# Optimization experiments

Measured on AMD Instinct MI355X. Metric: run time of the kernel, lower is better.

The kernel has to match this reference:

```python
import jax, jax.numpy as jnp
import numpy as np

EMBED = 1024
HEADS = 16


def setup_inputs() -> dict:
    key = jax.random.key(0)
    k1, k2, k3 = jax.random.split(key, 3)
    B, S, D = 2, 2048, EMBED
    x = jax.random.normal(k1, (B, S, D), dtype=jnp.float32)
    # nn.Linear weights: stored as [out, in]; y = x @ W.T
    w_qkv = jax.random.normal(k2, (3 * D, D), dtype=jnp.float32) * (D ** -0.5)
    w_out = jax.random.normal(k3, (D, D), dtype=jnp.float32) * (D ** -0.5)
    return {"x": x, "w_qkv": w_qkv, "w_out": w_out}


def reference(x, w_qkv, w_out):
    B, S, D = x.shape
    H = HEADS
    hd = D // H
    qkv = x @ w_qkv.T                       # [B, S, 3D]
    q, k, v = jnp.split(qkv, 3, axis=-1)
    # 'b l (head k) -> b head l k'
    def heads(t):
        return t.reshape(B, S, H, hd).transpose(0, 2, 1, 3)
    q, k, v = heads(q), heads(k), heads(v)
    scale = hd ** 0.5
    scores = jnp.einsum('bhqd,bhkd->bhqk', q, k) / scale
    probs = jax.nn.softmax(scores, axis=-1)
    out = jnp.einsum('bhqk,bhkd->bhqd', probs, v)  # [B, H, S, hd]
    out = out.transpose(0, 2, 1, 3).reshape(B, S, D)
    return out @ w_out.T
```

## Files before the change

### kernel.cpp

```cpp
#include <hip/hip_runtime.h>

typedef short short8 __attribute__((ext_vector_type(8)));
typedef float floatx4 __attribute__((ext_vector_type(4)));
typedef unsigned short ushort_t;

#define EMBED 1024
#define HEADS 16
#define HD 64
#define SEQ 2048
#define BATCH 2

__device__ inline ushort_t f2bf(float f) {
    unsigned int u = __float_as_uint(f);
    u += 0x7fff + ((u >> 16) & 1);
    return (ushort_t)(u >> 16);
}

typedef const __attribute__((address_space(1))) unsigned int* gas_t;
typedef __attribute__((address_space(3))) unsigned int* las_t;
__device__ inline void async_copy16(const ushort_t* g, ushort_t* l) {
    __builtin_amdgcn_global_load_lds((gas_t)g, (las_t)l, 16, 0, 0);
}

__global__ void cast3_kernel(const float* __restrict__ a, ushort_t* __restrict__ oa, int na,
                             const float* __restrict__ b, ushort_t* __restrict__ ob, int nb,
                             const float* __restrict__ c, ushort_t* __restrict__ oc, int nc) {
    int idx = (blockIdx.x * blockDim.x + threadIdx.x) * 4;
    const float* in; ushort_t* out;
    if (idx < na)            { in = a;  out = oa; }
    else if (idx < na + nb)  { in = b;  out = ob; idx -= na; }
    else if (idx < na + nb + nc) { in = c; out = oc; idx -= na + nb; }
    else return;
    float4 f = *(const float4*)(in + idx);
    ushort4 o;
    o.x = f2bf(f.x); o.y = f2bf(f.y); o.z = f2bf(f.z); o.w = f2bf(f.w);
    *(ushort4*)(out + idx) = o;
}

#define BM 128
#define BN 128
#define BK 32

template<int MODE>
__launch_bounds__(256, 3)
__global__ void gemm_bt(const ushort_t* __restrict__ A, const ushort_t* __restrict__ B,
                        float* __restrict__ outF,
                        ushort_t* __restrict__ qb, ushort_t* __restrict__ kb,
                        ushort_t* __restrict__ vtb,
                        int M, int N, int K) {
    __shared__ ushort_t As[BM * BK];
    __shared__ ushort_t Bs[BN * BK];
    const int t    = threadIdx.x;
    const int lane = t & 63;
    const int wave = t >> 6;
    const int wm   = (wave >> 1) * 64;
    const int wn   = (wave & 1) * 64;
    const int m0   = blockIdx.y * BM;
    const int n0   = blockIdx.x * BN;
    const int col  = lane & 15;
    const int quad = lane >> 4;

    const int srow = lane >> 2;
    const int sgr  = (lane & 3) ^ (srow & 3);
    const int rslot = quad ^ (col & 3);

    floatx4 acc[4][4] = {};

    for (int k0 = 0; k0 < K; k0 += BK) {
        for (int half = 0; half < 2; ++half) {
            int row0 = wave * 32 + half * 16;
            int r = row0 + srow;
            async_copy16(A + (size_t)(m0 + r) * K + k0 + sgr * 8, &As[row0 * BK]);
            async_copy16(B + (size_t)(n0 + r) * K + k0 + sgr * 8, &Bs[row0 * BK]);
        }
        __syncthreads();
        short8 a[4], b[4];
        for (int i = 0; i < 4; ++i)
            a[i] = *(const short8*)(&As[(wm + i * 16 + col) * BK + rslot * 8]);
        for (int j = 0; j < 4; ++j)
            b[j] = *(const short8*)(&Bs[(wn + j * 16 + col) * BK + rslot * 8]);
        for (int i = 0; i < 4; ++i)
            for (int j = 0; j < 4; ++j)
                acc[i][j] = __builtin_amdgcn_mfma_f32_16x16x32_bf16(a[i], b[j], acc[i][j], 0, 0, 0);
        __syncthreads();
    }

    for (int i = 0; i < 4; ++i)
        for (int j = 0; j < 4; ++j)
            for (int r = 0; r < 4; ++r) {
                int m = m0 + wm + i * 16 + quad * 4 + r;
                int n = n0 + wn + j * 16 + col;
                float c = acc[i][j][r];
                if (MODE == 1) {
                    outF[(size_t)m * N + n] = c;
                } else {
                    int part = n >> 10;
                    int within = n & 1023;
                    int h = within >> 6, d = within & 63;
                    int bb = m >> 11, s = m & 2047;
                    ushort_t v = f2bf(c);
                    if (part == 0)      qb [(((size_t)bb * HEADS + h) * SEQ + s) * HD + d] = v;
                    else if (part == 1) kb [(((size_t)bb * HEADS + h) * SEQ + s) * HD + d] = v;
                    else                vtb[(((size_t)bb * HEADS + h) * HD + d) * SEQ + s] = v;
                }
            }
}

#define LDP 72

__launch_bounds__(256, 3)
__global__ void attn_kernel(const ushort_t* __restrict__ qb, const ushort_t* __restrict__ kb,
                            const ushort_t* __restrict__ vtb, ushort_t* __restrict__ attn) {
    __shared__ ushort_t Klds[2][64 * 64];
    __shared__ ushort_t Vlds[2][64 * 64];
    __shared__ ushort_t Plds[4][2][16 * LDP];
    const int t    = threadIdx.x;
    const int lane = t & 63;
    const int wave = t >> 6;
    const int col  = lane & 15;
    const int quad = lane >> 4;
    const int bh   = blockIdx.y;
    const int q0   = blockIdx.x * 128 + wave * 32;

    const ushort_t* Q  = qb  + (size_t)bh * SEQ * HD;
    const ushort_t* Kp = kb  + (size_t)bh * SEQ * HD;
    const ushort_t* Vt = vtb + (size_t)bh * HD * SEQ;

    const int srow = lane >> 3;
    const int sgr  = lane & 7;

    short8 qf[2][2];
    for (int qt = 0; qt < 2; ++qt) {
        qf[qt][0] = *(const short8*)(Q + (size_t)(q0 + qt * 16 + col) * HD + quad * 8);
        qf[qt][1] = *(const short8*)(Q + (size_t)(q0 + qt * 16 + col) * HD + 32 + quad * 8);
    }

    floatx4 acc[2][4] = {};
    float lsum[2] = {0.f, 0.f};
    const float SC = 0.125f * 1.44269504f;
    const int sw = col & 7;

    auto stage = [&](int kt, int buf) {
        for (int inst = 0; inst < 2; ++inst) {
            int row0 = wave * 16 + inst * 8;
            int r = row0 + srow;
            const ushort_t* gk = Kp + (size_t)(kt + r) * HD + ((sgr ^ (r & 7)) * 8);
            async_copy16(gk, &Klds[buf][row0 * 64]);
            const ushort_t* gv = Vt + (size_t)r * SEQ + kt + ((sgr ^ (r & 7)) * 8);
            async_copy16(gv, &Vlds[buf][row0 * 64]);
        }
    };

    stage(0, 0);
    __syncthreads();

    for (int kt = 0; kt < SEQ; kt += 64) {
        const int cur = (kt >> 6) & 1;
        stage((kt + 64) & (SEQ - 1), cur ^ 1);

        const ushort_t* Kc = Klds[cur];
        const ushort_t* Vc = Vlds[cur];

        short8 kf[4][2];
        for (int n = 0; n < 4; ++n) {
            int row = n * 16 + col;
            kf[n][0] = *(const short8*)(Kc + row * 64 + ((quad ^ sw) * 8));
            kf[n][1] = *(const short8*)(Kc + row * 64 + (((4 + quad) ^ sw) * 8));
        }
        for (int qt = 0; qt < 2; ++qt)
            for (int n = 0; n < 4; ++n) {
                floatx4 z = {};
                z = __builtin_amdgcn_mfma_f32_16x16x32_bf16(kf[n][0], qf[qt][0], z, 0, 0, 0);
                z = __builtin_amdgcn_mfma_f32_16x16x32_bf16(kf[n][1], qf[qt][1], z, 0, 0, 0);
                unsigned int u0 = __float_as_uint(__builtin_amdgcn_exp2f(z[0] * SC));
                unsigned int u1 = __float_as_uint(__builtin_amdgcn_exp2f(z[1] * SC));
                unsigned int u2 = __float_as_uint(__builtin_amdgcn_exp2f(z[2] * SC));
                unsigned int u3 = __float_as_uint(__builtin_amdgcn_exp2f(z[3] * SC));
                lsum[qt] += (__uint_as_float(u0 & 0xffff0000u) + __uint_as_float(u1 & 0xffff0000u))
                          + (__uint_as_float(u2 & 0xffff0000u) + __uint_as_float(u3 & 0xffff0000u));
                uint2 pk;
                pk.x = __builtin_amdgcn_perm(u1, u0, 0x07060302u);
                pk.y = __builtin_amdgcn_perm(u3, u2, 0x07060302u);
                *(uint2*)(&Plds[wave][qt][col * LDP + n * 16 + quad * 4]) = pk;
            }
        short8 vf[4][2];
        for (int d = 0; d < 4; ++d) {
            int row = d * 16 + col;
            vf[d][0] = *(const short8*)(Vc + row * 64 + ((quad ^ sw) * 8));
            vf[d][1] = *(const short8*)(Vc + row * 64 + (((4 + quad) ^ sw) * 8));
        }
        for (int qt = 0; qt < 2; ++qt) {
            short8 pf0 = *(const short8*)(&Plds[wave][qt][col * LDP + quad * 8]);
            short8 pf1 = *(const short8*)(&Plds[wave][qt][col * LDP + 32 + quad * 8]);
            for (int d = 0; d < 4; ++d) {
                acc[qt][d] = __builtin_amdgcn_mfma_f32_16x16x32_bf16(pf0, vf[d][0], acc[qt][d], 0, 0, 0);
                acc[qt][d] = __builtin_amdgcn_mfma_f32_16x16x32_bf16(pf1, vf[d][1], acc[qt][d], 0, 0, 0);
            }
        }
        __syncthreads();
    }

    int b = bh >> 4, h = bh & 15;
    for (int qt = 0; qt < 2; ++qt) {
        float s = lsum[qt];
        s += __shfl_xor(s, 16);
        s += __shfl_xor(s, 32);
        float inv[4];
        for (int r = 0; r < 4; ++r)
            inv[r] = 1.0f / __shfl(s, quad * 4 + r);
        for (int d = 0; d < 4; ++d)
            for (int r = 0; r < 4; ++r) {
                int row = q0 + qt * 16 + quad * 4 + r;
                int cc  = h * HD + d * 16 + col;
                attn[((size_t)b * SEQ + row) * EMBED + cc] = f2bf(acc[qt][d][r] * inv[r]);
            }
    }
}

extern "C" void kernel_launch(void* const* d_in, const int* in_sizes, int n_in,
                              void* d_out, int out_size, void* d_ws, size_t ws_size,
                              hipStream_t stream) {
    const float* x     = (const float*)d_in[0];
    const float* w_qkv = (const float*)d_in[1];
    const float* w_out = (const float*)d_in[2];
    float* out = (float*)d_out;

    char* ws = (char*)d_ws;
    size_t off = 0;
    ushort_t* x_bf    = (ushort_t*)(ws + off); off += (size_t)BATCH * SEQ * EMBED * 2;
    ushort_t* wqkv_bf = (ushort_t*)(ws + off); off += (size_t)3 * EMBED * EMBED * 2;
    ushort_t* wout_bf = (ushort_t*)(ws + off); off += (size_t)EMBED * EMBED * 2;
    ushort_t* q_buf   = (ushort_t*)(ws + off); off += (size_t)BATCH * HEADS * SEQ * HD * 2;
    ushort_t* k_buf   = (ushort_t*)(ws + off); off += (size_t)BATCH * HEADS * SEQ * HD * 2;
    ushort_t* vt_buf  = (ushort_t*)(ws + off); off += (size_t)BATCH * HEADS * SEQ * HD * 2;
    ushort_t* attn_bf = (ushort_t*)(ws + off); off += (size_t)BATCH * SEQ * EMBED * 2;

    int n_x = BATCH * SEQ * EMBED, n_wq = 3 * EMBED * EMBED, n_wo = EMBED * EMBED;
    int n_all = n_x + n_wq + n_wo;
    cast3_kernel<<<n_all / 1024, 256, 0, stream>>>(x, x_bf, n_x, w_qkv, wqkv_bf, n_wq,
                                                   w_out, wout_bf, n_wo);

    gemm_bt<0><<<dim3(3 * EMBED / BN, BATCH * SEQ / BM), 256, 0, stream>>>(
        x_bf, wqkv_bf, nullptr, q_buf, k_buf, vt_buf, BATCH * SEQ, 3 * EMBED, EMBED);

    attn_kernel<<<dim3(SEQ / 128, BATCH * HEADS), 256, 0, stream>>>(q_buf, k_buf, vt_buf, attn_bf);

    gemm_bt<1><<<dim3(EMBED / BN, BATCH * SEQ / BM), 256, 0, stream>>>(
        attn_bf, wout_bf, out, nullptr, nullptr, nullptr, BATCH * SEQ, EMBED, EMBED);
}
```

Measured before the change: 199.1 us.

## Remap blocks for XCD-aware locality and halve attention query tile per wave

Both GEMMs and the attention kernel now use a 1D grid with a block-index remap. Consecutive IDs mod 8, which land on different XCDs, are assigned so that each XCD works on a contiguous group of M-tiles or heads, aiming for better L2 reuse of K/V and weights. The attention kernel also drops from 32 to 16 query rows per wave (64 per block), which doubles the grid to 1024 blocks and cuts registers and LDS. The cost is that each K/V tile loaded into LDS now feeds half as many MFMAs, so global and LDS traffic per unit of work rises.

Result: slower. 220.9 us (+11.0%).

```diff
diff --git a/kernel.cpp b/kernel.cpp
--- a/kernel.cpp
+++ b/kernel.cpp
@@ -50,13 +50,17 @@
                         int M, int N, int K) {
     __shared__ ushort_t As[BM * BK];
     __shared__ ushort_t Bs[BN * BK];
+    const int id   = blockIdx.x;
+    const int jj   = id >> 3;
+    const int bm   = (id & 7) * 4 + (jj & 3);
+    const int bn   = jj >> 2;
     const int t    = threadIdx.x;
     const int lane = t & 63;
     const int wave = t >> 6;
     const int wm   = (wave >> 1) * 64;
     const int wn   = (wave & 1) * 64;
-    const int m0   = blockIdx.y * BM;
-    const int n0   = blockIdx.x * BN;
+    const int m0   = bm * BM;
+    const int n0   = bn * BN;
     const int col  = lane & 15;
     const int quad = lane >> 4;
 
@@ -109,34 +113,34 @@
 #define LDP 72
 
 __launch_bounds__(256, 3)
-__global__ void attn_kernel(const ushort_t* __restrict__ qb, const ushort_t* __restrict__ kb,
+__global__ void attn_kernel(const ushort_t* __restrict__ qb_, const ushort_t* __restrict__ kb,
                             const ushort_t* __restrict__ vtb, ushort_t* __restrict__ attn) {
     __shared__ ushort_t Klds[2][64 * 64];
     __shared__ ushort_t Vlds[2][64 * 64];
-    __shared__ ushort_t Plds[4][2][16 * LDP];
+    __shared__ ushort_t Plds[4][16 * LDP];
+    const int id   = blockIdx.x;
+    const int jj   = id >> 3;
+    const int bh   = (id & 7) * 4 + (jj >> 5);
+    const int qblk = jj & 31;
     const int t    = threadIdx.x;
     const int lane = t & 63;
     const int wave = t >> 6;
     const int col  = lane & 15;
     const int quad = lane >> 4;
-    const int bh   = blockIdx.y;
-    const int q0   = blockIdx.x * 128 + wave * 32;
-
-    const ushort_t* Q  = qb  + (size_t)bh * SEQ * HD;
+    const int q0   = qblk * 64 + wave * 16;
+
+    const ushort_t* Q  = qb_ + (size_t)bh * SEQ * HD;
     const ushort_t* Kp = kb  + (size_t)bh * SEQ * HD;
     const ushort_t* Vt = vtb + (size_t)bh * HD * SEQ;
 
     const int srow = lane >> 3;
     const int sgr  = lane & 7;
 
-    short8 qf[2][2];
-    for (int qt = 0; qt < 2; ++qt) {
-        qf[qt][0] = *(const short8*)(Q + (size_t)(q0 + qt * 16 + col) * HD + quad * 8);
-        qf[qt][1] = *(const short8*)(Q + (size_t)(q0 + qt * 16 + col) * HD + 32 + quad * 8);
-    }
-
-    floatx4 acc[2][4] = {};
-    float lsum[2] = {0.f, 0.f};
+    short8 qf0 = *(const short8*)(Q + (size_t)(q0 + col) * HD + quad * 8);
+    short8 qf1 = *(const short8*)(Q + (size_t)(q0 + col) * HD + 32 + quad * 8);
+
+    floatx4 acc[4] = {};
+    float lsum = 0.f;
     const float SC = 0.125f * 1.44269504f;
     const int sw = col & 7;
 
@@ -167,54 +171,50 @@
             kf[n][0] = *(const short8*)(Kc + row * 64 + ((quad ^ sw) * 8));
             kf[n][1] = *(const short8*)(Kc + row * 64 + (((4 + quad) ^ sw) * 8));
         }
-        for (int qt = 0; qt < 2; ++qt)
-            for (int n = 0; n < 4; ++n) {
-                floatx4 z = {};
-                z = __builtin_amdgcn_mfma_f32_16x16x32_bf16(kf[n][0], qf[qt][0], z, 0, 0, 0);
-                z = __builtin_amdgcn_mfma_f32_16x16x32_bf16(kf[n][1], qf[qt][1], z, 0, 0, 0);
-                unsigned int u0 = __float_as_uint(__builtin_amdgcn_exp2f(z[0] * SC));
-                unsigned int u1 = __float_as_uint(__builtin_amdgcn_exp2f(z[1] * SC));
-                unsigned int u2 = __float_as_uint(__builtin_amdgcn_exp2f(z[2] * SC));
-                unsigned int u3 = __float_as_uint(__builtin_amdgcn_exp2f(z[3] * SC));
-                lsum[qt] += (__uint_as_float(u0 & 0xffff0000u) + __uint_as_float(u1 & 0xffff0000u))
-                          + (__uint_as_float(u2 & 0xffff0000u) + __uint_as_float(u3 & 0xffff0000u));
-                uint2 pk;
-                pk.x = __builtin_amdgcn_perm(u1, u0, 0x07060302u);
-                pk.y = __builtin_amdgcn_perm(u3, u2, 0x07060302u);
-                *(uint2*)(&Plds[wave][qt][col * LDP + n * 16 + quad * 4]) = pk;
-            }
+        for (int n = 0; n < 4; ++n) {
+            floatx4 z = {};
+            z = __builtin_amdgcn_mfma_f32_16x16x32_bf16(kf[n][0], qf0, z, 0, 0, 0);
+            z = __builtin_amdgcn_mfma_f32_16x16x32_bf16(kf[n][1], qf1, z, 0, 0, 0);
+            unsigned int u0 = __float_as_uint(__builtin_amdgcn_exp2f(z[0] * SC));
+            unsigned int u1 = __float_as_uint(__builtin_amdgcn_exp2f(z[1] * SC));
+            unsigned int u2 = __float_as_uint(__builtin_amdgcn_exp2f(z[2] * SC));
+            unsigned int u3 = __float_as_uint(__builtin_amdgcn_exp2f(z[3] * SC));
+            lsum += (__uint_as_float(u0 & 0xffff0000u) + __uint_as_float(u1 & 0xffff0000u))
+                  + (__uint_as_float(u2 & 0xffff0000u) + __uint_as_float(u3 & 0xffff0000u));
+            uint2 pk;
+            pk.x = __builtin_amdgcn_perm(u1, u0, 0x07060302u);
+            pk.y = __builtin_amdgcn_perm(u3, u2, 0x07060302u);
+            *(uint2*)(&Plds[wave][col * LDP + n * 16 + quad * 4]) = pk;
+        }
         short8 vf[4][2];
         for (int d = 0; d < 4; ++d) {
             int row = d * 16 + col;
             vf[d][0] = *(const short8*)(Vc + row * 64 + ((quad ^ sw) * 8));
             vf[d][1] = *(const short8*)(Vc + row * 64 + (((4 + quad) ^ sw) * 8));
         }
-        for (int qt = 0; qt < 2; ++qt) {
-            short8 pf0 = *(const short8*)(&Plds[wave][qt][col * LDP + quad * 8]);
-            short8 pf1 = *(const short8*)(&Plds[wave][qt][col * LDP + 32 + quad * 8]);
-            for (int d = 0; d < 4; ++d) {
-                acc[qt][d] = __builtin_amdgcn_mfma_f32_16x16x32_bf16(pf0, vf[d][0], acc[qt][d], 0, 0, 0);
-                acc[qt][d] = __builtin_amdgcn_mfma_f32_16x16x32_bf16(pf1, vf[d][1], acc[qt][d], 0, 0, 0);
-            }
+        short8 pf0 = *(const short8*)(&Plds[wave][col * LDP + quad * 8]);
+        short8 pf1 = *(const short8*)(&Plds[wave][col * LDP + 32 + quad * 8]);
+        for (int d = 0; d < 4; ++d) {
+            acc[d] = __builtin_amdgcn_mfma_f32_16x16x32_bf16(pf0, vf[d][0], acc[d], 0, 0, 0);
+            acc[d] = __builtin_amdgcn_mfma_f32_16x16x32_bf16(pf1, vf[d][1], acc[d], 0, 0, 0);
         }
         __syncthreads();
     }
 
+    float s = lsum;
+    s += __shfl_xor(s, 16);
+    s += __shfl_xor(s, 32);
+    float inv[4];
+    for (int r = 0; r < 4; ++r)
+        inv[r] = 1.0f / __shfl(s, quad * 4 + r);
+
     int b = bh >> 4, h = bh & 15;
-    for (int qt = 0; qt < 2; ++qt) {
-        float s = lsum[qt];
-        s += __shfl_xor(s, 16);
-        s += __shfl_xor(s, 32);
-        float inv[4];
-        for (int r = 0; r < 4; ++r)
-            inv[r] = 1.0f / __shfl(s, quad * 4 + r);
-        for (int d = 0; d < 4; ++d)
-            for (int r = 0; r < 4; ++r) {
-                int row = q0 + qt * 16 + quad * 4 + r;
-                int cc  = h * HD + d * 16 + col;
-                attn[((size_t)b * SEQ + row) * EMBED + cc] = f2bf(acc[qt][d][r] * inv[r]);
-            }
-    }
+    for (int d = 0; d < 4; ++d)
+        for (int r = 0; r < 4; ++r) {
+            int row = q0 + quad * 4 + r;
+            int cc  = h * HD + d * 16 + col;
+            attn[((size_t)b * SEQ + row) * EMBED + cc] = f2bf(acc[d][r] * inv[r]);
+        }
 }
 
 extern "C" void kernel_launch(void* const* d_in, const int* in_sizes, int n_in,
@@ -240,11 +240,11 @@
     cast3_kernel<<<n_all / 1024, 256, 0, stream>>>(x, x_bf, n_x, w_qkv, wqkv_bf, n_wq,
                                                    w_out, wout_bf, n_wo);
 
-    gemm_bt<0><<<dim3(3 * EMBED / BN, BATCH * SEQ / BM), 256, 0, stream>>>(
+    gemm_bt<0><<<768, 256, 0, stream>>>(
         x_bf, wqkv_bf, nullptr, q_buf, k_buf, vt_buf, BATCH * SEQ, 3 * EMBED, EMBED);
 
-    attn_kernel<<<dim3(SEQ / 128, BATCH * HEADS), 256, 0, stream>>>(q_buf, k_buf, vt_buf, attn_bf);
-
-    gemm_bt<1><<<dim3(EMBED / BN, BATCH * SEQ / BM), 256, 0, stream>>>(
+    attn_kernel<<<1024, 256, 0, stream>>>(q_buf, k_buf, vt_buf, attn_bf);
+
+    gemm_bt<1><<<256, 256, 0, stream>>>(
         attn_bf, wout_bf, out, nullptr, nullptr, nullptr, BATCH * SEQ, EMBED, EMBED);
 }
```

## Double GEMM K-tile, remap blocks for XCD-local L2 reuse, vectorize V^T stores

Applied to the files above, without the earlier changes.

Raises the GEMM K-tile from 32 to 64 with an 8-way LDS swizzle, which halves the number of barrier-separated loop iterations. Both GEMMs and the attention kernel move to a 1D grid whose block-index decode groups tiles that share A rows or a head onto the same XCD, aiming to improve L2 hit rates. The transposed V store in the QKV epilogue now writes four consecutive sequence positions as one 8-byte vector instead of four scattered 2-byte stores. The larger tile doubles LDS use per block and may reduce occupancy.

New measurement: 177.8 us. 10.7% less time.

```diff
diff --git a/kernel.cpp b/kernel.cpp
--- a/kernel.cpp
+++ b/kernel.cpp
@@ -1,6 +1,7 @@
 #include <hip/hip_runtime.h>
 
 typedef short short8 __attribute__((ext_vector_type(8)));
+typedef short short4v __attribute__((ext_vector_type(4)));
 typedef float floatx4 __attribute__((ext_vector_type(4)));
 typedef unsigned short ushort_t;
 
@@ -39,7 +40,7 @@
 
 #define BM 128
 #define BN 128
-#define BK 32
+#define BK 64
 
 template<int MODE>
 __launch_bounds__(256, 3)
@@ -50,79 +51,98 @@
                         int M, int N, int K) {
     __shared__ ushort_t As[BM * BK];
     __shared__ ushort_t Bs[BN * BK];
+    const int id   = blockIdx.x;
+    const int jj   = id >> 3;
+    const int bm   = (id & 7) * 4 + (jj & 3);
+    const int bn   = jj >> 2;
     const int t    = threadIdx.x;
     const int lane = t & 63;
     const int wave = t >> 6;
     const int wm   = (wave >> 1) * 64;
     const int wn   = (wave & 1) * 64;
-    const int m0   = blockIdx.y * BM;
-    const int n0   = blockIdx.x * BN;
+    const int m0   = bm * BM;
+    const int n0   = bn * BN;
     const int col  = lane & 15;
     const int quad = lane >> 4;
 
-    const int srow = lane >> 2;
-    const int sgr  = (lane & 3) ^ (srow & 3);
-    const int rslot = quad ^ (col & 3);
+    const int srow = lane >> 3;
+    const int sgr  = (lane & 7) ^ (srow & 7);
+    const int slot0 = quad ^ (col & 7);
 
     floatx4 acc[4][4] = {};
 
     for (int k0 = 0; k0 < K; k0 += BK) {
-        for (int half = 0; half < 2; ++half) {
-            int row0 = wave * 32 + half * 16;
+        for (int half = 0; half < 4; ++half) {
+            int row0 = wave * 32 + half * 8;
             int r = row0 + srow;
             async_copy16(A + (size_t)(m0 + r) * K + k0 + sgr * 8, &As[row0 * BK]);
             async_copy16(B + (size_t)(n0 + r) * K + k0 + sgr * 8, &Bs[row0 * BK]);
         }
         __syncthreads();
-        short8 a[4], b[4];
-        for (int i = 0; i < 4; ++i)
-            a[i] = *(const short8*)(&As[(wm + i * 16 + col) * BK + rslot * 8]);
-        for (int j = 0; j < 4; ++j)
-            b[j] = *(const short8*)(&Bs[(wn + j * 16 + col) * BK + rslot * 8]);
-        for (int i = 0; i < 4; ++i)
-            for (int j = 0; j < 4; ++j)
-                acc[i][j] = __builtin_amdgcn_mfma_f32_16x16x32_bf16(a[i], b[j], acc[i][j], 0, 0, 0);
+        short8 a[2][4], b[2][4];
+        for (int i = 0; i < 4; ++i) {
+            int base = (wm + i * 16 + col) * BK;
+            a[0][i] = *(const short8*)(&As[base + slot0 * 8]);
+            a[1][i] = *(const short8*)(&As[base + (slot0 ^ 4) * 8]);
+        }
+        for (int j = 0; j < 4; ++j) {
+            int base = (wn + j * 16 + col) * BK;
+            b[0][j] = *(const short8*)(&Bs[base + slot0 * 8]);
+            b[1][j] = *(const short8*)(&Bs[base + (slot0 ^ 4) * 8]);
+        }
+        for (int kk = 0; kk < 2; ++kk)
+            for (int i = 0; i < 4; ++i)
+                for (int j = 0; j < 4; ++j)
+                    acc[i][j] = __builtin_amdgcn_mfma_f32_16x16x32_bf16(a[kk][i], b[kk][j], acc[i][j], 0, 0, 0);
         __syncthreads();
     }
 
     for (int i = 0; i < 4; ++i)
-        for (int j = 0; j < 4; ++j)
-            for (int r = 0; r < 4; ++r) {
-                int m = m0 + wm + i * 16 + quad * 4 + r;
-                int n = n0 + wn + j * 16 + col;
-                float c = acc[i][j][r];
-                if (MODE == 1) {
-                    outF[(size_t)m * N + n] = c;
+        for (int j = 0; j < 4; ++j) {
+            int n = n0 + wn + j * 16 + col;
+            int mb = m0 + wm + i * 16 + quad * 4;
+            if (MODE == 1) {
+                for (int r = 0; r < 4; ++r)
+                    outF[(size_t)(mb + r) * N + n] = acc[i][j][r];
+            } else {
+                int part = n >> 10;
+                int within = n & 1023;
+                int h = within >> 6, d = within & 63;
+                int bb = mb >> 11, s = mb & 2047;
+                if (part == 2) {
+                    short4v pv;
+                    pv.x = (short)f2bf(acc[i][j][0]); pv.y = (short)f2bf(acc[i][j][1]);
+                    pv.z = (short)f2bf(acc[i][j][2]); pv.w = (short)f2bf(acc[i][j][3]);
+                    *(short4v*)(vtb + (((size_t)bb * HEADS + h) * HD + d) * SEQ + s) = pv;
                 } else {
-                    int part = n >> 10;
-                    int within = n & 1023;
-                    int h = within >> 6, d = within & 63;
-                    int bb = m >> 11, s = m & 2047;
-                    ushort_t v = f2bf(c);
-                    if (part == 0)      qb [(((size_t)bb * HEADS + h) * SEQ + s) * HD + d] = v;
-                    else if (part == 1) kb [(((size_t)bb * HEADS + h) * SEQ + s) * HD + d] = v;
-                    else                vtb[(((size_t)bb * HEADS + h) * HD + d) * SEQ + s] = v;
+                    ushort_t* dst = (part == 0) ? qb : kb;
+                    for (int r = 0; r < 4; ++r)
+                        dst[(((size_t)bb * HEADS + h) * SEQ + s + r) * HD + d] = f2bf(acc[i][j][r]);
                 }
             }
+        }
 }
 
 #define LDP 72
 
 __launch_bounds__(256, 3)
-__global__ void attn_kernel(const ushort_t* __restrict__ qb, const ushort_t* __restrict__ kb,
+__global__ void attn_kernel(const ushort_t* __restrict__ qb_, const ushort_t* __restrict__ kb,
                             const ushort_t* __restrict__ vtb, ushort_t* __restrict__ attn) {
     __shared__ ushort_t Klds[2][64 * 64];
     __shared__ ushort_t Vlds[2][64 * 64];
     __shared__ ushort_t Plds[4][2][16 * LDP];
+    const int id   = blockIdx.x;
+    const int jj   = id >> 3;
+    const int bh   = (id & 7) * 4 + (jj >> 4);
+    const int qblk = jj & 15;
     const int t    = threadIdx.x;
     const int lane = t & 63;
     const int wave = t >> 6;
     const int col  = lane & 15;
     const int quad = lane >> 4;
-    const int bh   = blockIdx.y;
-    const int q0   = blockIdx.x * 128 + wave * 32;
-
-    const ushort_t* Q  = qb  + (size_t)bh * SEQ * HD;
+    const int q0   = qblk * 128 + wave * 32;
+
+    const ushort_t* Q  = qb_ + (size_t)bh * SEQ * HD;
     const ushort_t* Kp = kb  + (size_t)bh * SEQ * HD;
     const ushort_t* Vt = vtb + (size_t)bh * HD * SEQ;
 
@@ -240,11 +260,11 @@
     cast3_kernel<<<n_all / 1024, 256, 0, stream>>>(x, x_bf, n_x, w_qkv, wqkv_bf, n_wq,
                                                    w_out, wout_bf, n_wo);
 
-    gemm_bt<0><<<dim3(3 * EMBED / BN, BATCH * SEQ / BM), 256, 0, stream>>>(
+    gemm_bt<0><<<768, 256, 0, stream>>>(
         x_bf, wqkv_bf, nullptr, q_buf, k_buf, vt_buf, BATCH * SEQ, 3 * EMBED, EMBED);
 
-    attn_kernel<<<dim3(SEQ / 128, BATCH * HEADS), 256, 0, stream>>>(q_buf, k_buf, vt_buf, attn_bf);
-
-    gemm_bt<1><<<dim3(EMBED / BN, BATCH * SEQ / BM), 256, 0, stream>>>(
+    attn_kernel<<<512, 256, 0, stream>>>(q_buf, k_buf, vt_buf, attn_bf);
+
+    gemm_bt<1><<<256, 256, 0, stream>>>(
         attn_bf, wout_bf, out, nullptr, nullptr, nullptr, BATCH * SEQ, EMBED, EMBED);
 }
```
